# Optimization experiments

Measured on AMD Instinct MI355X. Metric: run time of the kernel, lower is better.

## Reference

```python
import jax, jax.numpy as jnp
import numpy as np

N_NODES = 20000
D = 8


def setup_inputs() -> dict:
    key = jax.random.key(0)
    k1, k2, k3 = jax.random.split(key, 3)
    E_half = 250000
    src = jax.random.randint(k1, (E_half,), 0, N_NODES, dtype=jnp.int32)
    dst = jax.random.randint(k2, (E_half,), 0, N_NODES, dtype=jnp.int32)
    # builder expects both edge directions present (symmetric edge set)
    row = jnp.concatenate([src, dst])
    col = jnp.concatenate([dst, src])
    edge_index = jnp.stack([row, col])  # (2, 500000) int32
    E = row.shape[0]
    restriction_maps = jax.random.normal(k3, (E, D, D), dtype=jnp.float32)
    return {"restriction_maps": restriction_maps, "edge_index": edge_index}


def _sheaf_adjacency_values(restriction_maps, edge_index, n=N_NODES):
    """Faithful port of SheafAdjacencyBuilder: transport maps + sparse values
    with self-loops and symmetric normalization. Returns the normalized sparse
    value vector of length (E + n) * d * d (off-diagonal blocks then diagonal)."""
    row, col = edge_index[0], edge_index[1]
    E = row.shape[0]
    d = restriction_maps.shape[-1]
    # --- reverse-edge lookup via hashed searchsorted (matches torch source) ---
    eh = row * n + col              # fits int32 for n=20000
    rh = col * n + row
    order = jnp.argsort(eh)
    sorted_h = eh[order]
    pos = jnp.clip(jnp.searchsorted(sorted_h, rh), 0, E - 1)
    rev = jnp.where(sorted_h[pos] == rh, order[pos], jnp.arange(E, dtype=order.dtype))
    # --- per-edge transport maps P_ij = F_src^T @ F_dst, shape (E, d, d) ---
    P = jnp.einsum('eji,ejk->eik', restriction_maps, restriction_maps[rev])
    # --- sparse block indices ---
    dr = jnp.arange(d, dtype=jnp.int32)
    off_row = jnp.broadcast_to(row[:, None, None] * d + dr[None, :, None], (E, d, d)).reshape(-1)
    off_col = jnp.broadcast_to(col[:, None, None] * d + dr[None, None, :], (E, d, d)).reshape(-1)
    node_base = jnp.arange(n, dtype=jnp.int32) * d
    diag_row = jnp.broadcast_to(node_base[:, None, None] + dr[None, :, None], (n, d, d)).reshape(-1)
    diag_col = jnp.broadcast_to(node_base[:, None, None] + dr[None, None, :], (n, d, d)).reshape(-1)
    eye_vals = jnp.broadcast_to(jnp.eye(d, dtype=restriction_maps.dtype), (n, d, d)).reshape(-1)
    rows = jnp.concatenate([off_row, diag_row])
    cols = jnp.concatenate([off_col, diag_col])
    vals = jnp.concatenate([P.reshape(-1), eye_vals])
    # --- symmetric normalization D^{-1/2} A D^{-1/2} (deg of |values|) ---
    Nd = n * d
    deg = jax.ops.segment_sum(jnp.abs(vals), rows, num_segments=Nd)
    deg_safe = jnp.where(deg > 0, deg, 1.0)
    dinv = jnp.where(deg > 0, deg_safe ** -0.5, 0.0)
    return dinv[rows] * vals * dinv[cols]


def reference(restriction_maps, edge_index):
    return _sheaf_adjacency_values(restriction_maps, edge_index)
```

## Files before the change

kernel.cpp:

```cpp
#include <hip/hip_runtime.h>
#include <stdint.h>

constexpr int NN   = 20000;
constexpr int DD   = 8;
constexpr int ND   = NN * DD;
constexpr uint32_t HSIZE = 1u << 20;
constexpr uint32_t HMASK = HSIZE - 1;
constexpr unsigned long long EMPTY64 = ~0ULL;

typedef float v4f __attribute__((ext_vector_type(4)));

__device__ __forceinline__ uint32_t hkey(uint32_t k) {
    k *= 2654435761u;
    return k ^ (k >> 15);
}

__device__ __forceinline__ int hprobe(const unsigned long long* __restrict__ slots,
                                      uint32_t key, int fallback) {
    uint32_t s = hkey(key) & HMASK;
    while (true) {
        unsigned long long v = slots[s];
        if (v == EMPTY64) return fallback;
        if ((uint32_t)(v >> 19) == key) return (int)(v & 0x7FFFFu);
        s = (s + 1) & HMASK;
    }
}

__device__ __forceinline__ void mac8(const float* __restrict__ fav,
                                     const float* __restrict__ fbv,
                                     int i, float* __restrict__ acc) {
#pragma unroll
    for (int j = 0; j < 8; ++j) {
        float  a  = fav[j * 8 + i];
        float4 b0 = *(const float4*)&fbv[j * 8];
        float4 b1 = *(const float4*)&fbv[j * 8 + 4];
        acc[0] = fmaf(a, b0.x, acc[0]);  acc[1] = fmaf(a, b0.y, acc[1]);
        acc[2] = fmaf(a, b0.z, acc[2]);  acc[3] = fmaf(a, b0.w, acc[3]);
        acc[4] = fmaf(a, b1.x, acc[4]);  acc[5] = fmaf(a, b1.y, acc[5]);
        acc[6] = fmaf(a, b1.z, acc[6]);  acc[7] = fmaf(a, b1.w, acc[7]);
    }
}

__global__ void k_fill(unsigned long long* __restrict__ slots,
                       float* __restrict__ deg) {
    uint32_t i = blockIdx.x * blockDim.x + threadIdx.x;
    if (i < HSIZE / 2) {
        ulonglong2 v; v.x = EMPTY64; v.y = EMPTY64;
        ((ulonglong2*)slots)[i] = v;
    }
    if (i < (uint32_t)ND) deg[i] = 1.0f;
}

__global__ void k_insert(const int* __restrict__ row, const int* __restrict__ col,
                         unsigned long long* __restrict__ slots, int E) {
    int e = blockIdx.x * blockDim.x + threadIdx.x;
    if (e >= E) return;
    uint32_t key = (uint32_t)(row[e] * NN + col[e]);
    unsigned long long cur = ((unsigned long long)key << 19) | (unsigned)e;
    uint32_t s = hkey(key) & HMASK;
    while (true) {
        unsigned long long old = atomicMin(&slots[s], cur);
        if (old == EMPTY64) break;
        if ((uint32_t)(old >> 19) == key) break;
        if (old > cur) { cur = old; key = (uint32_t)(cur >> 19); }
        s = (s + 1) & HMASK;
    }
}

__global__ void __launch_bounds__(256)
k_deg(const float* __restrict__ F,
      const int* __restrict__ row, const int* __restrict__ col,
      const unsigned long long* __restrict__ slots, int* __restrict__ task,
      float* __restrict__ deg, int E, int EH) {
    __shared__ float fa[64 * 68];
    __shared__ int s_x[64], s_me[64], s_f[64], s_cls[64], s_row[64], s_col[64];
    const int t  = threadIdx.x;
    const int b0 = blockIdx.x * 32;

    if (t < 64) {
        int s = t;
        int x = (s < 32) ? (b0 + s) : (EH + b0 + (s - 32));
        bool valid = (s < 32) ? (x < EH) : (x < E);
        int r = 0, c = 0, me = -1;
        if (valid) {
            r = row[x]; c = col[x];
            me = hprobe(slots, (uint32_t)(r * NN + c), x);
        } else x = -1;
        s_x[s] = x; s_row[s] = r; s_col[s] = c; s_me[s] = me;
    }
    __syncthreads();

    if (t < 64) {
        int s = t, x = s_x[s];
        int cls = 0, f = 0;
        if (x >= 0) {
            int q = s ^ 32;
            int r = s_row[s], c = s_col[s], me = s_me[s];
            if (s_x[q] >= 0 && s_row[q] == c && s_col[q] == r) f = s_me[q];
            else f = hprobe(slots, (uint32_t)(c * NN + r), x);
            cls = (f == x) ? 1 : ((me == x) ? ((x < f) ? 2 : 0) : 1);
            task[x] = f | (cls << 29);
        }
        s_f[s] = f; s_cls[s] = cls;
    }

    const float4* F4 = (const float4*)F;
#pragma unroll
    for (int p = 0; p < 4; ++p) {
        int q = t + p * 256;
        int sl = q >> 4, sub = q & 15;
        int x = s_x[sl];
        if (x >= 0)
            *(float4*)&fa[sl * 68 + (sub << 2)] = F4[(size_t)x * 16 + sub];
    }
    __syncthreads();

    const int g = t >> 3, i = t & 7;
#pragma unroll
    for (int item = 0; item < 2; ++item) {
        int s = (item == 0) ? g : (g + 32);
        int q = s ^ 32;
        int x = s_x[s];
        int cls = (x >= 0) ? s_cls[s] : 0;
        if (cls) {
            int f = s_f[s];
            const float* fav = &fa[s * 68];
            float acc[8] = {0,0,0,0,0,0,0,0};
            const float* lsrc = (f == s_x[q]) ? &fa[q * 68] : ((f == x) ? fav : nullptr);
            if (lsrc) mac8(fav, lsrc, i, acc);
            else      mac8(fav, F + (size_t)f * 64, i, acc);
            float b0f=fabsf(acc[0]),b1=fabsf(acc[1]),b2=fabsf(acc[2]),b3=fabsf(acc[3]);
            float b4=fabsf(acc[4]),b5=fabsf(acc[5]),b6=fabsf(acc[6]),b7=fabsf(acc[7]);
            atomicAdd(&deg[s_row[s] * DD + i], b0f+b1+b2+b3+b4+b5+b6+b7);
            if (cls == 2) {
#pragma unroll
                for (int m = 1; m < 8; m <<= 1) {
                    b0f+=__shfl_xor(b0f,m); b1+=__shfl_xor(b1,m);
                    b2 +=__shfl_xor(b2,m);  b3+=__shfl_xor(b3,m);
                    b4 +=__shfl_xor(b4,m);  b5+=__shfl_xor(b5,m);
                    b6 +=__shfl_xor(b6,m);  b7+=__shfl_xor(b7,m);
                }
                float ci = (i&4) ? ((i&2)?((i&1)?b7:b6):((i&1)?b5:b4))
                                 : ((i&2)?((i&1)?b3:b2):((i&1)?b1:b0f));
                atomicAdd(&deg[s_col[s] * DD + i], ci);
            }
        }
    }
}

__global__ void __launch_bounds__(256)
k_pnorm(const float* __restrict__ F,
        const int* __restrict__ row, const int* __restrict__ col,
        const int* __restrict__ task, const float* __restrict__ deg,
        float* __restrict__ out, int E, int EH, int NB) {
    const int t = threadIdx.x;

    if ((int)blockIdx.x >= NB) {
        int r = (blockIdx.x - NB) * 256 + t;
        if (r >= ND) return;
        float dd = 1.0f / deg[r];
        int i = r & 7;
        v4f a = { 0.f, 0.f, 0.f, 0.f };
        v4f b = { 0.f, 0.f, 0.f, 0.f };
        if (i < 4) a[i] = dd; else b[i - 4] = dd;
        size_t base = (size_t)E * 64 + (size_t)(r >> 3) * 64 + (size_t)i * 8;
        *(v4f*)&out[base]     = a;
        *(v4f*)&out[base + 4] = b;
        return;
    }

    __shared__ float fa[64 * 68];
    __shared__ int s_x[64], s_f[64], s_cls[64], s_row[64], s_col[64];
    const int b0 = blockIdx.x * 32;

    if (t < 64) {
        int s = t;
        int x = (s < 32) ? (b0 + s) : (EH + b0 + (s - 32));
        bool valid = (s < 32) ? (x < EH) : (x < E);
        int cls = 0, f = 0, r = 0, c = 0;
        if (valid) {
            int w = task[x];
            cls = w >> 29;
            f   = w & ((1 << 29) - 1);
            r = row[x]; c = col[x];
        } else x = -1;
        s_x[s] = x; s_f[s] = f; s_cls[s] = cls; s_row[s] = r; s_col[s] = c;
    }
    __syncthreads();

    const float4* F4 = (const float4*)F;
#pragma unroll
    for (int p = 0; p < 4; ++p) {
        int q = t + p * 256;
        int sl = q >> 4, sub = q & 15;
        int x = s_x[sl];
        if (x >= 0)
            *(float4*)&fa[sl * 68 + (sub << 2)] = F4[(size_t)x * 16 + sub];
    }
    __syncthreads();

    const int g = t >> 3, i = t & 7;
#pragma unroll
    for (int item = 0; item < 2; ++item) {
        int s = (item == 0) ? g : (g + 32);
        int q = s ^ 32;
        int x = s_x[s];
        int cls = (x >= 0) ? s_cls[s] : 0;
        if (cls) {
            int f = s_f[s];
            const float* fav = &fa[s * 68];
            float acc[8] = {0,0,0,0,0,0,0,0};
            const float* lsrc = (f == s_x[q]) ? &fa[q * 68] : ((f == x) ? fav : nullptr);
            if (lsrc) mac8(fav, lsrc, i, acc);
            else      mac8(fav, F + (size_t)f * 64, i, acc);

            const int r = s_row[s], c = s_col[s];
            float dr = 1.0f / sqrtf(deg[r * DD + i]);
            v4f dg0 = *(const v4f*)&deg[c * DD];
            v4f dg1 = *(const v4f*)&deg[c * DD + 4];
            v4f dc0, dc1;
            dc0.x = 1.0f / sqrtf(dg0.x);  dc0.y = 1.0f / sqrtf(dg0.y);
            dc0.z = 1.0f / sqrtf(dg0.z);  dc0.w = 1.0f / sqrtf(dg0.w);
            dc1.x = 1.0f / sqrtf(dg1.x);  dc1.y = 1.0f / sqrtf(dg1.y);
            dc1.z = 1.0f / sqrtf(dg1.z);  dc1.w = 1.0f / sqrtf(dg1.w);

            float v[8];
            v[0]=acc[0]*dr*dc0.x; v[1]=acc[1]*dr*dc0.y;
            v[2]=acc[2]*dr*dc0.z; v[3]=acc[3]*dr*dc0.w;
            v[4]=acc[4]*dr*dc1.x; v[5]=acc[5]*dr*dc1.y;
            v[6]=acc[6]*dr*dc1.z; v[7]=acc[7]*dr*dc1.w;

            v4f w0 = { v[0], v[1], v[2], v[3] };
            v4f w1 = { v[4], v[5], v[6], v[7] };
            size_t ob = (size_t)x * 64 + i * 8;
            *(v4f*)&out[ob]     = w0;
            *(v4f*)&out[ob + 4] = w1;

            if (cls == 2) {
#pragma unroll
                for (int m = 1; m < 8; m <<= 1) {
#pragma unroll
                    for (int j = 0; j < 8; ++j) {
                        if ((j & m) == 0) {
                            float sel = (i & m) ? v[j] : v[j | m];
                            float got = __shfl_xor(sel, m);
                            float nj  = (i & m) ? got : v[j];
                            float njm = (i & m) ? v[j | m] : got;
                            v[j] = nj;  v[j | m] = njm;
                        }
                    }
                }
                v4f u0 = { v[0], v[1], v[2], v[3] };
                v4f u1 = { v[4], v[5], v[6], v[7] };
                size_t fb_ = (size_t)f * 64 + i * 8;
                *(v4f*)&out[fb_]     = u0;
                *(v4f*)&out[fb_ + 4] = u1;
            }
        }
    }
}

extern "C" void kernel_launch(void* const* d_in, const int* in_sizes, int n_in,
                              void* d_out, int out_size, void* d_ws, size_t ws_size,
                              hipStream_t stream) {
    const float* F  = (const float*)d_in[0];
    const int*   ei = (const int*)d_in[1];
    const int E = in_sizes[1] / 2;
    const int* row = ei;
    const int* col = ei + E;
    const int EH = E / 2;
    const int NB = ((E - EH) + 31) / 32;
    const int NDIAG = (ND + 255) / 256;

    unsigned long long* slots = (unsigned long long*)d_ws;
    int*   task = (int*)(slots + HSIZE);
    float* deg  = (float*)(task + E);
    float* out  = (float*)d_out;

    k_fill  <<<(HSIZE / 2 + 255) / 256, 256, 0, stream>>>(slots, deg);
    k_insert<<<(E + 255) / 256,  256, 0, stream>>>(row, col, slots, E);
    k_deg   <<<NB,               256, 0, stream>>>(F, row, col, slots, task, deg, E, EH);
    k_pnorm <<<NB + NDIAG,       256, 0, stream>>>(F, row, col, task, deg, out, E, EH, NB);
}
```

Baseline: 141.4 us.

## Merge four kernels into one persistent cooperative kernel with grid syncs

```diff
diff --git a/kernel.cpp b/kernel.cpp
--- a/kernel.cpp
+++ b/kernel.cpp
@@ -1,5 +1,8 @@
 #include <hip/hip_runtime.h>
+#include <hip/hip_cooperative_groups.h>
 #include <stdint.h>
+
+namespace cg = cooperative_groups;
 
 constexpr int NN   = 20000;
 constexpr int DD   = 8;
@@ -41,222 +44,214 @@
     }
 }
 
-__global__ void k_fill(unsigned long long* __restrict__ slots,
-                       float* __restrict__ deg) {
-    uint32_t i = blockIdx.x * blockDim.x + threadIdx.x;
-    if (i < HSIZE / 2) {
+__global__ void __launch_bounds__(256)
+k_mega(const float* __restrict__ F,
+       const int* __restrict__ row, const int* __restrict__ col,
+       unsigned long long* __restrict__ slots, int* __restrict__ task,
+       float* __restrict__ deg, float* __restrict__ out,
+       int E, int EH, int NB, int NT) {
+    cg::grid_group grid = cg::this_grid();
+    const int t    = threadIdx.x;
+    const int nblk = gridDim.x;
+    const int gth  = nblk * 256;
+
+    __shared__ float fa[64 * 68];
+    __shared__ int s_x[64], s_me[64], s_f[64], s_cls[64], s_row[64], s_col[64];
+
+    for (uint32_t i = blockIdx.x * 256 + t; i < HSIZE / 2; i += gth) {
         ulonglong2 v; v.x = EMPTY64; v.y = EMPTY64;
         ((ulonglong2*)slots)[i] = v;
     }
-    if (i < (uint32_t)ND) deg[i] = 1.0f;
-}
-
-__global__ void k_insert(const int* __restrict__ row, const int* __restrict__ col,
-                         unsigned long long* __restrict__ slots, int E) {
-    int e = blockIdx.x * blockDim.x + threadIdx.x;
-    if (e >= E) return;
-    uint32_t key = (uint32_t)(row[e] * NN + col[e]);
-    unsigned long long cur = ((unsigned long long)key << 19) | (unsigned)e;
-    uint32_t s = hkey(key) & HMASK;
-    while (true) {
-        unsigned long long old = atomicMin(&slots[s], cur);
-        if (old == EMPTY64) break;
-        if ((uint32_t)(old >> 19) == key) break;
-        if (old > cur) { cur = old; key = (uint32_t)(cur >> 19); }
-        s = (s + 1) & HMASK;
-    }
-}
-
-__global__ void __launch_bounds__(256)
-k_deg(const float* __restrict__ F,
-      const int* __restrict__ row, const int* __restrict__ col,
-      const unsigned long long* __restrict__ slots, int* __restrict__ task,
-      float* __restrict__ deg, int E, int EH) {
-    __shared__ float fa[64 * 68];
-    __shared__ int s_x[64], s_me[64], s_f[64], s_cls[64], s_row[64], s_col[64];
-    const int t  = threadIdx.x;
-    const int b0 = blockIdx.x * 32;
-
-    if (t < 64) {
-        int s = t;
-        int x = (s < 32) ? (b0 + s) : (EH + b0 + (s - 32));
-        bool valid = (s < 32) ? (x < EH) : (x < E);
-        int r = 0, c = 0, me = -1;
-        if (valid) {
-            r = row[x]; c = col[x];
-            me = hprobe(slots, (uint32_t)(r * NN + c), x);
-        } else x = -1;
-        s_x[s] = x; s_row[s] = r; s_col[s] = c; s_me[s] = me;
-    }
-    __syncthreads();
-
-    if (t < 64) {
-        int s = t, x = s_x[s];
-        int cls = 0, f = 0;
-        if (x >= 0) {
+    for (int i = blockIdx.x * 256 + t; i < ND; i += gth) deg[i] = 1.0f;
+    grid.sync();
+
+    for (int e = blockIdx.x * 256 + t; e < E; e += gth) {
+        uint32_t key = (uint32_t)(row[e] * NN + col[e]);
+        unsigned long long cur = ((unsigned long long)key << 19) | (unsigned)e;
+        uint32_t s = hkey(key) & HMASK;
+        while (true) {
+            unsigned long long old = atomicMin(&slots[s], cur);
+            if (old == EMPTY64) break;
+            if ((uint32_t)(old >> 19) == key) break;
+            if (old > cur) { cur = old; key = (uint32_t)(cur >> 19); }
+            s = (s + 1) & HMASK;
+        }
+    }
+    grid.sync();
+
+    const float4* F4 = (const float4*)F;
+    for (int tile = blockIdx.x; tile < NB; tile += nblk) {
+        const int b0 = tile * 32;
+        if (t < 64) {
+            int s = t;
+            int x = (s < 32) ? (b0 + s) : (EH + b0 + (s - 32));
+            bool valid = (s < 32) ? (x < EH) : (x < E);
+            int r = 0, c = 0, me = -1;
+            if (valid) {
+                r = row[x]; c = col[x];
+                me = hprobe(slots, (uint32_t)(r * NN + c), x);
+            } else x = -1;
+            s_x[s] = x; s_row[s] = r; s_col[s] = c; s_me[s] = me;
+        }
+        __syncthreads();
+        if (t < 64) {
+            int s = t, x = s_x[s];
+            int cls = 0, f = 0;
+            if (x >= 0) {
+                int q = s ^ 32;
+                int r = s_row[s], c = s_col[s], me = s_me[s];
+                if (s_x[q] >= 0 && s_row[q] == c && s_col[q] == r) f = s_me[q];
+                else f = hprobe(slots, (uint32_t)(c * NN + r), x);
+                cls = (f == x) ? 1 : ((me == x) ? ((x < f) ? 2 : 0) : 1);
+                task[x] = f | (cls << 29);
+            }
+            s_f[s] = f; s_cls[s] = cls;
+        }
+#pragma unroll
+        for (int p = 0; p < 4; ++p) {
+            int q = t + p * 256;
+            int sl = q >> 4, sub = q & 15;
+            int x = s_x[sl];
+            if (x >= 0)
+                *(float4*)&fa[sl * 68 + (sub << 2)] = F4[(size_t)x * 16 + sub];
+        }
+        __syncthreads();
+
+        const int g = t >> 3, i = t & 7;
+#pragma unroll
+        for (int item = 0; item < 2; ++item) {
+            int s = (item == 0) ? g : (g + 32);
             int q = s ^ 32;
-            int r = s_row[s], c = s_col[s], me = s_me[s];
-            if (s_x[q] >= 0 && s_row[q] == c && s_col[q] == r) f = s_me[q];
-            else f = hprobe(slots, (uint32_t)(c * NN + r), x);
-            cls = (f == x) ? 1 : ((me == x) ? ((x < f) ? 2 : 0) : 1);
-            task[x] = f | (cls << 29);
-        }
-        s_f[s] = f; s_cls[s] = cls;
-    }
-
-    const float4* F4 = (const float4*)F;
-#pragma unroll
-    for (int p = 0; p < 4; ++p) {
-        int q = t + p * 256;
-        int sl = q >> 4, sub = q & 15;
-        int x = s_x[sl];
-        if (x >= 0)
-            *(float4*)&fa[sl * 68 + (sub << 2)] = F4[(size_t)x * 16 + sub];
-    }
-    __syncthreads();
-
-    const int g = t >> 3, i = t & 7;
-#pragma unroll
-    for (int item = 0; item < 2; ++item) {
-        int s = (item == 0) ? g : (g + 32);
-        int q = s ^ 32;
-        int x = s_x[s];
-        int cls = (x >= 0) ? s_cls[s] : 0;
-        if (cls) {
-            int f = s_f[s];
-            const float* fav = &fa[s * 68];
-            float acc[8] = {0,0,0,0,0,0,0,0};
-            const float* lsrc = (f == s_x[q]) ? &fa[q * 68] : ((f == x) ? fav : nullptr);
-            if (lsrc) mac8(fav, lsrc, i, acc);
-            else      mac8(fav, F + (size_t)f * 64, i, acc);
-            float b0f=fabsf(acc[0]),b1=fabsf(acc[1]),b2=fabsf(acc[2]),b3=fabsf(acc[3]);
-            float b4=fabsf(acc[4]),b5=fabsf(acc[5]),b6=fabsf(acc[6]),b7=fabsf(acc[7]);
-            atomicAdd(&deg[s_row[s] * DD + i], b0f+b1+b2+b3+b4+b5+b6+b7);
-            if (cls == 2) {
-#pragma unroll
-                for (int m = 1; m < 8; m <<= 1) {
-                    b0f+=__shfl_xor(b0f,m); b1+=__shfl_xor(b1,m);
-                    b2 +=__shfl_xor(b2,m);  b3+=__shfl_xor(b3,m);
-                    b4 +=__shfl_xor(b4,m);  b5+=__shfl_xor(b5,m);
-                    b6 +=__shfl_xor(b6,m);  b7+=__shfl_xor(b7,m);
+            int x = s_x[s];
+            int cls = (x >= 0) ? s_cls[s] : 0;
+            if (cls) {
+                int f = s_f[s];
+                const float* fav = &fa[s * 68];
+                float acc[8] = {0,0,0,0,0,0,0,0};
+                const float* lsrc = (f == s_x[q]) ? &fa[q * 68] : ((f == x) ? fav : nullptr);
+                if (lsrc) mac8(fav, lsrc, i, acc);
+                else      mac8(fav, F + (size_t)f * 64, i, acc);
+                float b0f=fabsf(acc[0]),b1=fabsf(acc[1]),b2=fabsf(acc[2]),b3=fabsf(acc[3]);
+                float b4=fabsf(acc[4]),b5=fabsf(acc[5]),b6=fabsf(acc[6]),b7=fabsf(acc[7]);
+                atomicAdd(&deg[s_row[s] * DD + i], b0f+b1+b2+b3+b4+b5+b6+b7);
+                if (cls == 2) {
+#pragma unroll
+                    for (int m = 1; m < 8; m <<= 1) {
+                        b0f+=__shfl_xor(b0f,m); b1+=__shfl_xor(b1,m);
+                        b2 +=__shfl_xor(b2,m);  b3+=__shfl_xor(b3,m);
+                        b4 +=__shfl_xor(b4,m);  b5+=__shfl_xor(b5,m);
+                        b6 +=__shfl_xor(b6,m);  b7+=__shfl_xor(b7,m);
+                    }
+                    float ci = (i&4) ? ((i&2)?((i&1)?b7:b6):((i&1)?b5:b4))
+                                     : ((i&2)?((i&1)?b3:b2):((i&1)?b1:b0f));
+                    atomicAdd(&deg[s_col[s] * DD + i], ci);
                 }
-                float ci = (i&4) ? ((i&2)?((i&1)?b7:b6):((i&1)?b5:b4))
-                                 : ((i&2)?((i&1)?b3:b2):((i&1)?b1:b0f));
-                atomicAdd(&deg[s_col[s] * DD + i], ci);
-            }
-        }
-    }
-}
-
-__global__ void __launch_bounds__(256)
-k_pnorm(const float* __restrict__ F,
-        const int* __restrict__ row, const int* __restrict__ col,
-        const int* __restrict__ task, const float* __restrict__ deg,
-        float* __restrict__ out, int E, int EH, int NB) {
-    const int t = threadIdx.x;
-
-    if ((int)blockIdx.x >= NB) {
-        int r = (blockIdx.x - NB) * 256 + t;
-        if (r >= ND) return;
-        float dd = 1.0f / deg[r];
-        int i = r & 7;
-        v4f a = { 0.f, 0.f, 0.f, 0.f };
-        v4f b = { 0.f, 0.f, 0.f, 0.f };
-        if (i < 4) a[i] = dd; else b[i - 4] = dd;
-        size_t base = (size_t)E * 64 + (size_t)(r >> 3) * 64 + (size_t)i * 8;
-        *(v4f*)&out[base]     = a;
-        *(v4f*)&out[base + 4] = b;
-        return;
-    }
-
-    __shared__ float fa[64 * 68];
-    __shared__ int s_x[64], s_f[64], s_cls[64], s_row[64], s_col[64];
-    const int b0 = blockIdx.x * 32;
-
-    if (t < 64) {
-        int s = t;
-        int x = (s < 32) ? (b0 + s) : (EH + b0 + (s - 32));
-        bool valid = (s < 32) ? (x < EH) : (x < E);
-        int cls = 0, f = 0, r = 0, c = 0;
-        if (valid) {
-            int w = task[x];
-            cls = w >> 29;
-            f   = w & ((1 << 29) - 1);
-            r = row[x]; c = col[x];
-        } else x = -1;
-        s_x[s] = x; s_f[s] = f; s_cls[s] = cls; s_row[s] = r; s_col[s] = c;
-    }
-    __syncthreads();
-
-    const float4* F4 = (const float4*)F;
-#pragma unroll
-    for (int p = 0; p < 4; ++p) {
-        int q = t + p * 256;
-        int sl = q >> 4, sub = q & 15;
-        int x = s_x[sl];
-        if (x >= 0)
-            *(float4*)&fa[sl * 68 + (sub << 2)] = F4[(size_t)x * 16 + sub];
-    }
-    __syncthreads();
-
-    const int g = t >> 3, i = t & 7;
-#pragma unroll
-    for (int item = 0; item < 2; ++item) {
-        int s = (item == 0) ? g : (g + 32);
-        int q = s ^ 32;
-        int x = s_x[s];
-        int cls = (x >= 0) ? s_cls[s] : 0;
-        if (cls) {
-            int f = s_f[s];
-            const float* fav = &fa[s * 68];
-            float acc[8] = {0,0,0,0,0,0,0,0};
-            const float* lsrc = (f == s_x[q]) ? &fa[q * 68] : ((f == x) ? fav : nullptr);
-            if (lsrc) mac8(fav, lsrc, i, acc);
-            else      mac8(fav, F + (size_t)f * 64, i, acc);
-
-            const int r = s_row[s], c = s_col[s];
-            float dr = 1.0f / sqrtf(deg[r * DD + i]);
-            v4f dg0 = *(const v4f*)&deg[c * DD];
-            v4f dg1 = *(const v4f*)&deg[c * DD + 4];
-            v4f dc0, dc1;
-            dc0.x = 1.0f / sqrtf(dg0.x);  dc0.y = 1.0f / sqrtf(dg0.y);
-            dc0.z = 1.0f / sqrtf(dg0.z);  dc0.w = 1.0f / sqrtf(dg0.w);
-            dc1.x = 1.0f / sqrtf(dg1.x);  dc1.y = 1.0f / sqrtf(dg1.y);
-            dc1.z = 1.0f / sqrtf(dg1.z);  dc1.w = 1.0f / sqrtf(dg1.w);
-
-            float v[8];
-            v[0]=acc[0]*dr*dc0.x; v[1]=acc[1]*dr*dc0.y;
-            v[2]=acc[2]*dr*dc0.z; v[3]=acc[3]*dr*dc0.w;
-            v[4]=acc[4]*dr*dc1.x; v[5]=acc[5]*dr*dc1.y;
-            v[6]=acc[6]*dr*dc1.z; v[7]=acc[7]*dr*dc1.w;
-
-            v4f w0 = { v[0], v[1], v[2], v[3] };
-            v4f w1 = { v[4], v[5], v[6], v[7] };
-            size_t ob = (size_t)x * 64 + i * 8;
-            *(v4f*)&out[ob]     = w0;
-            *(v4f*)&out[ob + 4] = w1;
-
-            if (cls == 2) {
-#pragma unroll
-                for (int m = 1; m < 8; m <<= 1) {
-#pragma unroll
-                    for (int j = 0; j < 8; ++j) {
-                        if ((j & m) == 0) {
-                            float sel = (i & m) ? v[j] : v[j | m];
-                            float got = __shfl_xor(sel, m);
-                            float nj  = (i & m) ? got : v[j];
-                            float njm = (i & m) ? v[j | m] : got;
-                            v[j] = nj;  v[j | m] = njm;
+            }
+        }
+        __syncthreads();
+    }
+    grid.sync();
+
+    for (int tile = blockIdx.x; tile < NT; tile += nblk) {
+        if (tile >= NB) {
+            int r = (tile - NB) * 256 + t;
+            if (r < ND) {
+                float dd = 1.0f / deg[r];
+                int i = r & 7;
+                v4f a = { 0.f, 0.f, 0.f, 0.f };
+                v4f b = { 0.f, 0.f, 0.f, 0.f };
+                if (i < 4) a[i] = dd; else b[i - 4] = dd;
+                size_t base = (size_t)E * 64 + (size_t)(r >> 3) * 64 + (size_t)i * 8;
+                *(v4f*)&out[base]     = a;
+                *(v4f*)&out[base + 4] = b;
+            }
+            continue;
+        }
+        const int b0 = tile * 32;
+        if (t < 64) {
+            int s = t;
+            int x = (s < 32) ? (b0 + s) : (EH + b0 + (s - 32));
+            bool valid = (s < 32) ? (x < EH) : (x < E);
+            int cls = 0, f = 0, r = 0, c = 0;
+            if (valid) {
+                int w = task[x];
+                cls = w >> 29;
+                f   = w & ((1 << 29) - 1);
+                r = row[x]; c = col[x];
+            } else x = -1;
+            s_x[s] = x; s_f[s] = f; s_cls[s] = cls; s_row[s] = r; s_col[s] = c;
+        }
+        __syncthreads();
+#pragma unroll
+        for (int p = 0; p < 4; ++p) {
+            int q = t + p * 256;
+            int sl = q >> 4, sub = q & 15;
+            int x = s_x[sl];
+            if (x >= 0)
+                *(float4*)&fa[sl * 68 + (sub << 2)] = F4[(size_t)x * 16 + sub];
+        }
+        __syncthreads();
+
+        const int g = t >> 3, i = t & 7;
+#pragma unroll
+        for (int item = 0; item < 2; ++item) {
+            int s = (item == 0) ? g : (g + 32);
+            int q = s ^ 32;
+            int x = s_x[s];
+            int cls = (x >= 0) ? s_cls[s] : 0;
+            if (cls) {
+                int f = s_f[s];
+                const float* fav = &fa[s * 68];
+                float acc[8] = {0,0,0,0,0,0,0,0};
+                const float* lsrc = (f == s_x[q]) ? &fa[q * 68] : ((f == x) ? fav : nullptr);
+                if (lsrc) mac8(fav, lsrc, i, acc);
+                else      mac8(fav, F + (size_t)f * 64, i, acc);
+
+                const int r = s_row[s], c = s_col[s];
+                float dr = 1.0f / sqrtf(deg[r * DD + i]);
+                v4f dg0 = *(const v4f*)&deg[c * DD];
+                v4f dg1 = *(const v4f*)&deg[c * DD + 4];
+                v4f dc0, dc1;
+                dc0.x = 1.0f / sqrtf(dg0.x);  dc0.y = 1.0f / sqrtf(dg0.y);
+                dc0.z = 1.0f / sqrtf(dg0.z);  dc0.w = 1.0f / sqrtf(dg0.w);
+                dc1.x = 1.0f / sqrtf(dg1.x);  dc1.y = 1.0f / sqrtf(dg1.y);
+                dc1.z = 1.0f / sqrtf(dg1.z);  dc1.w = 1.0f / sqrtf(dg1.w);
+
+                float v[8];
+                v[0]=acc[0]*dr*dc0.x; v[1]=acc[1]*dr*dc0.y;
+                v[2]=acc[2]*dr*dc0.z; v[3]=acc[3]*dr*dc0.w;
+                v[4]=acc[4]*dr*dc1.x; v[5]=acc[5]*dr*dc1.y;
+                v[6]=acc[6]*dr*dc1.z; v[7]=acc[7]*dr*dc1.w;
+
+                v4f w0 = { v[0], v[1], v[2], v[3] };
+                v4f w1 = { v[4], v[5], v[6], v[7] };
+                size_t ob = (size_t)x * 64 + i * 8;
+                *(v4f*)&out[ob]     = w0;
+                *(v4f*)&out[ob + 4] = w1;
+
+                if (cls == 2) {
+#pragma unroll
+                    for (int m = 1; m < 8; m <<= 1) {
+#pragma unroll
+                        for (int j = 0; j < 8; ++j) {
+                            if ((j & m) == 0) {
+                                float sel = (i & m) ? v[j] : v[j | m];
+                                float got = __shfl_xor(sel, m);
+                                float nj  = (i & m) ? got : v[j];
+                                float njm = (i & m) ? v[j | m] : got;
+                                v[j] = nj;  v[j | m] = njm;
+                            }
                         }
                     }
+                    v4f u0 = { v[0], v[1], v[2], v[3] };
+                    v4f u1 = { v[4], v[5], v[6], v[7] };
+                    size_t fb_ = (size_t)f * 64 + i * 8;
+                    *(v4f*)&out[fb_]     = u0;
+                    *(v4f*)&out[fb_ + 4] = u1;
                 }
-                v4f u0 = { v[0], v[1], v[2], v[3] };
-                v4f u1 = { v[4], v[5], v[6], v[7] };
-                size_t fb_ = (size_t)f * 64 + i * 8;
-                *(v4f*)&out[fb_]     = u0;
-                *(v4f*)&out[fb_ + 4] = u1;
-            }
-        }
+            }
+        }
+        __syncthreads();
     }
 }
 
@@ -265,20 +260,30 @@
                               hipStream_t stream) {
     const float* F  = (const float*)d_in[0];
     const int*   ei = (const int*)d_in[1];
-    const int E = in_sizes[1] / 2;
+    int E = in_sizes[1] / 2;
     const int* row = ei;
     const int* col = ei + E;
-    const int EH = E / 2;
-    const int NB = ((E - EH) + 31) / 32;
-    const int NDIAG = (ND + 255) / 256;
+    int EH = E / 2;
+    int NB = ((E - EH) + 31) / 32;
+    int NT = NB + (ND + 255) / 256;
 
     unsigned long long* slots = (unsigned long long*)d_ws;
     int*   task = (int*)(slots + HSIZE);
     float* deg  = (float*)(task + E);
     float* out  = (float*)d_out;
 
-    k_fill  <<<(HSIZE / 2 + 255) / 256, 256, 0, stream>>>(slots, deg);
-    k_insert<<<(E + 255) / 256,  256, 0, stream>>>(row, col, slots, E);
-    k_deg   <<<NB,               256, 0, stream>>>(F, row, col, slots, task, deg, E, EH);
-    k_pnorm <<<NB + NDIAG,       256, 0, stream>>>(F, row, col, task, deg, out, E, EH, NB);
-}
+    int dev = 0;
+    hipGetDevice(&dev);
+    hipDeviceProp_t prop;
+    hipGetDeviceProperties(&prop, dev);
+    int perCU = 0;
+    hipOccupancyMaxActiveBlocksPerMultiprocessor(&perCU, (const void*)k_mega, 256, 0);
+    if (perCU < 1) perCU = 1;
+    int grid = perCU * prop.multiProcessorCount;
+    if (grid > NT) grid = NT;
+
+    void* args[] = { (void*)&F, (void*)&row, (void*)&col, (void*)&slots,
+                     (void*)&task, (void*)&deg, (void*)&out,
+                     (void*)&E, (void*)&EH, (void*)&NB, (void*)&NT };
+    hipLaunchCooperativeKernel((void*)k_mega, dim3(grid), dim3(256), args, 0, stream);
+}
```

New measurement: 410.5 us. +190.4%, slower.
